# Performance work log

Hardware: AMD Instinct MI355X
Metric: run time of the kernel (lower is better)

The kernel has to match this reference:

```python
import jax, jax.numpy as jnp
import numpy as np

N = 100000
E = 3200000
F_IN = 128
H1, C1 = 2, 16          # conv1: heads=2, out_channels=16, concat -> 32
H2, C2 = 1, 40          # conv2: heads=1, out_channels=num_classes=40
NEG_SLOPE = 0.2


def setup_inputs() -> dict:
    key = jax.random.key(0)
    ks = jax.random.split(key, 12)
    features = jax.random.normal(ks[0], (N, F_IN), dtype=jnp.float32)
    edges = jax.random.randint(ks[1], (2, E), 0, N, dtype=jnp.int64)
    weight = jax.random.uniform(ks[2], (E,), dtype=jnp.float32)  # ignored (edge_dim=None)
    s = 0.1
    W1 = jax.random.normal(ks[3], (F_IN, H1 * C1), dtype=jnp.float32) * s
    att_src1 = jax.random.normal(ks[4], (H1, C1), dtype=jnp.float32) * s
    att_dst1 = jax.random.normal(ks[5], (H1, C1), dtype=jnp.float32) * s
    b1 = jnp.zeros((H1 * C1,), dtype=jnp.float32)
    W2 = jax.random.normal(ks[6], (H1 * C1, H2 * C2), dtype=jnp.float32) * s
    att_src2 = jax.random.normal(ks[7], (H2, C2), dtype=jnp.float32) * s
    att_dst2 = jax.random.normal(ks[8], (H2, C2), dtype=jnp.float32) * s
    b2 = jnp.zeros((H2 * C2,), dtype=jnp.float32)
    return {"features": features, "edges": edges, "weight": weight,
            "W1": W1, "att_src1": att_src1, "att_dst1": att_dst1, "b1": b1,
            "W2": W2, "att_src2": att_src2, "att_dst2": att_dst2, "b2": b2}


def _segment_softmax(e, seg, num_segments):
    # e: [E, H]; softmax over edges sharing the same destination node
    m = jax.ops.segment_max(e, seg, num_segments=num_segments)
    ex = jnp.exp(e - m[seg])
    s = jax.ops.segment_sum(ex, seg, num_segments=num_segments)
    return ex / (s[seg] + 1e-16)


def _gat_conv(x, src, dst, W, att_src, att_dst, bias, heads, out_ch):
    n = x.shape[0]
    h = (x @ W).reshape(n, heads, out_ch)                  # [N,H,C]
    a_src = jnp.sum(h * att_src, axis=-1)                  # [N,H]
    a_dst = jnp.sum(h * att_dst, axis=-1)                  # [N,H]
    e = a_src[src] + a_dst[dst]                            # [E,H]
    e = jnp.where(e > 0, e, NEG_SLOPE * e)                 # LeakyReLU(0.2)
    alpha = _segment_softmax(e, dst, n)                    # [E,H]
    msg = h[src] * alpha[:, :, None]                       # [E,H,C]
    out = jax.ops.segment_sum(msg, dst, num_segments=n)    # [N,H,C]
    return out.reshape(n, heads * out_ch) + bias           # concat=True


def reference(features, edges, weight, W1, att_src1, att_dst1, b1,
              W2, att_src2, att_dst2, b2):
    n = features.shape[0]
    # GATConv default add_self_loops=True (self-loop removal of pre-existing
    # loops skipped: negligible for random edges and not jit-shape-friendly)
    loop = jnp.arange(n, dtype=edges.dtype)
    src = jnp.concatenate([edges[0], loop])
    dst = jnp.concatenate([edges[1], loop])
    x = _gat_conv(features, src, dst, W1, att_src1, att_dst1, b1, H1, C1)
    x = jax.nn.relu(x)
    # F.dropout with training=self.training -> identity in eval mode
    x = _gat_conv(x, src, dst, W2, att_src2, att_dst2, b2, H2, C2)
    return x
```

## Files before the change

kernel.cpp:

```cpp
#include <hip/hip_runtime.h>


#define DEVFN __device__ __forceinline__
#define CB_SHIFT 8
#define CB_SZ 256
#define SC_CHUNK 4096
#define NBMAX 512
#define STASH 12288

DEVFN unsigned short f2h(float f) {
  _Float16 h = (_Float16)f;
  unsigned short u;
  __builtin_memcpy(&u, &h, 2);
  return u;
}
DEVFN float h2f(unsigned short u) {
  _Float16 h;
  __builtin_memcpy(&h, &u, 2);
  return (float)h;
}

DEVFN float lrelu(float e) { return e > 0.f ? e : 0.2f * e; }

DEVFN void acc8(float* acc, float x, uint4 u) {
  acc[0] = fmaf(x, h2f(u.x & 0xffff), acc[0]);
  acc[1] = fmaf(x, h2f(u.x >> 16),    acc[1]);
  acc[2] = fmaf(x, h2f(u.y & 0xffff), acc[2]);
  acc[3] = fmaf(x, h2f(u.y >> 16),    acc[3]);
  acc[4] = fmaf(x, h2f(u.z & 0xffff), acc[4]);
  acc[5] = fmaf(x, h2f(u.z >> 16),    acc[5]);
  acc[6] = fmaf(x, h2f(u.w & 0xffff), acc[6]);
  acc[7] = fmaf(x, h2f(u.w >> 16),    acc[7]);
}

DEVFN void read_edge(const long long* eg64, const int* eg32, int is64, int E,
                     int i, int& s, int& d) {
  if (i >= E) { s = d = i - E; return; }
  if (is64) { s = (int)eg64[i]; d = (int)eg64[E + i]; }
  else      { s = eg32[i];      d = eg32[E + i]; }
}

DEVFN int detect64(const int* eg32, int E, int i0, int t) {
  int base = i0;
  if (base > E - 64) base = E - 64;
  if (base < 0) base = 0;
  int i = base + (t & 63);
  unsigned long long m = __ballot((i < E) && (eg32[2 * i + 1] != 0));
  return m == 0ull;
}

__global__ __launch_bounds__(256) void bucket_hist(const long long* eg64,
                                                   const int* eg32,
                                                   int E, int N, int NB2,
                                                   int* __restrict__ bhist) {
  __shared__ int lh[NBMAX];
  int t = threadIdx.x;
  lh[t] = 0; lh[t + 256] = 0;
  int is64 = detect64(eg32, E, 0, t);
  __syncthreads();
  int EN = E + N;
  int step = (int)gridDim.x * 1024;
  for (int base = (int)blockIdx.x * 1024; base < EN; base += step) {
#pragma unroll
    for (int k = 0; k < 4; k++) {
      int i = base + k * 256 + t;
      if (i < EN) {
        int d;
        if (i >= E) d = i - E;
        else d = is64 ? (int)eg64[E + i] : eg32[E + i];
        atomicAdd(&lh[d >> CB_SHIFT], 1);
      }
    }
  }
  __syncthreads();
  if (t < NB2 && lh[t]) atomicAdd(&bhist[t], lh[t]);
  int t2 = t + 256;
  if (t2 < NB2 && lh[t2]) atomicAdd(&bhist[t2], lh[t2]);
}

__global__ void bucket_scan(const int* __restrict__ bhist,
                            int* __restrict__ bscan, int* __restrict__ gcur,
                            int NB2, int EN) {
  __shared__ int buf[2][NBMAX];
  int t = threadIdx.x;
  int v = (t < NB2) ? bhist[t] : 0;
  buf[0][t] = v;
  __syncthreads();
  int pin = 0;
  for (int off = 1; off < NBMAX; off <<= 1) {
    int nv = buf[pin][t] + (t >= off ? buf[pin][t - off] : 0);
    buf[1 - pin][t] = nv;
    pin ^= 1;
    __syncthreads();
  }
  int excl = buf[pin][t] - v;
  if (t < NB2) { bscan[t] = excl; gcur[t] = excl; }
  if (t == NB2) bscan[t] = EN;
}

__global__ __launch_bounds__(256) void chunk_scatter_sorted(
    const long long* eg64, const int* eg32, int E, int N, int NB2,
    int* __restrict__ gcur, int* __restrict__ tmp) {
  __shared__ int lh[NBMAX];
  __shared__ int lscan[NBMAX];
  __shared__ int lpos[NBMAX];
  __shared__ int gbase[NBMAX];
  __shared__ int sbuf[2][NBMAX];
  __shared__ int payl[SC_CHUNK];
  __shared__ unsigned short bktid[SC_CHUNK];
  int t = threadIdx.x;
  int i0 = (int)blockIdx.x * SC_CHUNK;
  int is64 = detect64(eg32, E, i0, t);
  lh[t] = 0; lh[t + 256] = 0;
  __syncthreads();
  int EN = E + N;
  int i1 = i0 + SC_CHUNK; if (i1 > EN) i1 = EN;
  int total = i1 - i0;
  int es[16], ed[16];
#pragma unroll
  for (int bb = 0; bb < 4; bb++) {
#pragma unroll
    for (int k = 0; k < 4; k++) {
      int idx = bb * 4 + k;
      int i = i0 + bb * 1024 + k * 256 + t;
      int s = 0, d = -1;
      if (i < i1) read_edge(eg64, eg32, is64, E, i, s, d);
      es[idx] = s; ed[idx] = d;
    }
  }
#pragma unroll
  for (int j = 0; j < 16; j++)
    if (ed[j] >= 0) atomicAdd(&lh[ed[j] >> CB_SHIFT], 1);
  __syncthreads();
  sbuf[0][t] = lh[t]; sbuf[0][t + 256] = lh[t + 256];
  __syncthreads();
  int pin = 0;
  for (int off = 1; off < NBMAX; off <<= 1) {
    int nv0 = sbuf[pin][t] + (t >= off ? sbuf[pin][t - off] : 0);
    int nv1 = sbuf[pin][t + 256] + sbuf[pin][t + 256 - off];
    __syncthreads();
    sbuf[1 - pin][t] = nv0; sbuf[1 - pin][t + 256] = nv1;
    pin ^= 1;
    __syncthreads();
  }
  lscan[t] = sbuf[pin][t] - lh[t];
  lscan[t + 256] = sbuf[pin][t + 256] - lh[t + 256];
  lpos[t] = lscan[t]; lpos[t + 256] = lscan[t + 256];
  if (t < NB2 && lh[t]) gbase[t] = atomicAdd(&gcur[t], lh[t]);
  int t2 = t + 256;
  if (t2 < NB2 && lh[t2]) gbase[t2] = atomicAdd(&gcur[t2], lh[t2]);
  __syncthreads();
#pragma unroll
  for (int j = 0; j < 16; j++) {
    if (ed[j] >= 0) {
      int b = ed[j] >> CB_SHIFT;
      int sl = atomicAdd(&lpos[b], 1);
      payl[sl] = (es[j] << CB_SHIFT) | (ed[j] & (CB_SZ - 1));
      bktid[sl] = (unsigned short)b;
    }
  }
  __syncthreads();
  for (int j = t; j < total; j += 256) {
    int b = bktid[j];
    tmp[gbase[b] + (j - lscan[b])] = payl[j];
  }
}

__global__ __launch_bounds__(256) void bucket_rp_sort(const int* __restrict__ bscan,
                                                      const int* __restrict__ tmp,
                                                      int* __restrict__ rp,
                                                      int* __restrict__ csr,
                                                      int N, int EN) {
  __shared__ int lc[CB_SZ];
  __shared__ int ps[256];
  __shared__ int lcur[CB_SZ];
  __shared__ int stash[STASH];
  int b = blockIdx.x, t = threadIdx.x;
  lc[t] = 0;
  __syncthreads();
  int w0 = bscan[b];
  int w1 = bscan[b + 1];
  int cnt = w1 - w0;
  bool fit = (cnt <= STASH);
  int p = w0 + t;
  for (; p + 768 < w1; p += 1024) {
    int e0 = tmp[p], e1 = tmp[p + 256], e2 = tmp[p + 512], e3 = tmp[p + 768];
    if (fit) {
      stash[p - w0] = e0; stash[p - w0 + 256] = e1;
      stash[p - w0 + 512] = e2; stash[p - w0 + 768] = e3;
    }
    atomicAdd(&lc[e0 & (CB_SZ - 1)], 1);
    atomicAdd(&lc[e1 & (CB_SZ - 1)], 1);
    atomicAdd(&lc[e2 & (CB_SZ - 1)], 1);
    atomicAdd(&lc[e3 & (CB_SZ - 1)], 1);
  }
  if (p < w1) {
    bool v1 = p + 256 < w1, v2 = p + 512 < w1;
    int q1 = v1 ? p + 256 : p;
    int q2 = v2 ? p + 512 : p;
    int e0 = tmp[p], e1 = tmp[q1], e2 = tmp[q2];
    if (fit) {
      stash[p - w0] = e0;
      if (v1) stash[q1 - w0] = e1;
      if (v2) stash[q2 - w0] = e2;
    }
    atomicAdd(&lc[e0 & (CB_SZ - 1)], 1);
    if (v1) atomicAdd(&lc[e1 & (CB_SZ - 1)], 1);
    if (v2) atomicAdd(&lc[e2 & (CB_SZ - 1)], 1);
  }
  __syncthreads();
  int a = lc[t];
  ps[t] = a;
  __syncthreads();
  for (int off = 1; off < 256; off <<= 1) {
    int v = ps[t];
    int u = (t >= off) ? ps[t - off] : 0;
    __syncthreads();
    ps[t] = v + u;
    __syncthreads();
  }
  int base = w0 + ps[t] - a;
  lcur[t] = base;
  int n0 = b * CB_SZ;
  if (n0 + t < N) rp[n0 + t] = base;
  if (b == (int)gridDim.x - 1 && t == 0) rp[N] = EN;
  __syncthreads();
  if (fit) {
    for (int j = t; j < cnt; j += 256) {
      int e = stash[j];
      int pos = atomicAdd(&lcur[e & (CB_SZ - 1)], 1);
      csr[pos] = e >> CB_SHIFT;
    }
  } else {
    for (int q = w0 + t; q < w1; q += 256) {
      int e = tmp[q];
      int pos = atomicAdd(&lcur[e & (CB_SZ - 1)], 1);
      csr[pos] = e >> CB_SHIFT;
    }
  }
}

__global__ __launch_bounds__(256) void gemm1f(const float* __restrict__ X,
                                              const float* __restrict__ W,
                                              const float* __restrict__ att_s,
                                              const float* __restrict__ att_d,
                                              uint4* __restrict__ h1h,
                                              float* __restrict__ as1,
                                              float* __restrict__ ad1, int N) {
  __shared__ float Wl[128 * 32];
  __shared__ float Asl[32], Adl[32];
  int t = threadIdx.x;
  for (int i = t; i < 1024; i += 256)
    ((float4*)Wl)[i] = ((const float4*)W)[i];
  if (t < 32) { Asl[t] = att_s[t]; Adl[t] = att_d[t]; }
  __syncthreads();
  int g = t >> 2, j = t & 3;
  int n0 = blockIdx.x * 128 + g * 2;
  int n1 = n0 + 1;
  bool v0 = n0 < N, v1 = n1 < N;
  const float4* X40 = (const float4*)(X + (size_t)n0 * 128);
  const float4* X41 = (const float4*)(X + (size_t)n1 * 128);
  float a0[8], a1[8];
#pragma unroll
  for (int c = 0; c < 8; c++) { a0[c] = 0.f; a1[c] = 0.f; }
  float4 z4 = {0.f, 0.f, 0.f, 0.f};
  for (int k4 = 0; k4 < 32; k4++) {
    float4 x0 = v0 ? X40[k4] : z4;
    float4 x1 = v1 ? X41[k4] : z4;
    const float4* w4 = (const float4*)(Wl + k4 * 128);
    int cb = j * 2;
#pragma unroll
    for (int kr = 0; kr < 4; kr++) {
      float4 wa = w4[kr * 8 + cb];
      float4 wb = w4[kr * 8 + cb + 1];
      float xc0 = kr == 0 ? x0.x : kr == 1 ? x0.y : kr == 2 ? x0.z : x0.w;
      float xc1 = kr == 0 ? x1.x : kr == 1 ? x1.y : kr == 2 ? x1.z : x1.w;
      a0[0] = fmaf(xc0, wa.x, a0[0]); a0[1] = fmaf(xc0, wa.y, a0[1]);
      a0[2] = fmaf(xc0, wa.z, a0[2]); a0[3] = fmaf(xc0, wa.w, a0[3]);
      a0[4] = fmaf(xc0, wb.x, a0[4]); a0[5] = fmaf(xc0, wb.y, a0[5]);
      a0[6] = fmaf(xc0, wb.z, a0[6]); a0[7] = fmaf(xc0, wb.w, a0[7]);
      a1[0] = fmaf(xc1, wa.x, a1[0]); a1[1] = fmaf(xc1, wa.y, a1[1]);
      a1[2] = fmaf(xc1, wa.z, a1[2]); a1[3] = fmaf(xc1, wa.w, a1[3]);
      a1[4] = fmaf(xc1, wb.x, a1[4]); a1[5] = fmaf(xc1, wb.y, a1[5]);
      a1[6] = fmaf(xc1, wb.z, a1[6]); a1[7] = fmaf(xc1, wb.w, a1[7]);
    }
  }
  int ch0 = j * 8;
  float ps0 = 0.f, pd0 = 0.f, ps1 = 0.f, pd1 = 0.f;
#pragma unroll
  for (int c = 0; c < 8; c++) {
    ps0 = fmaf(a0[c], Asl[ch0 + c], ps0);
    pd0 = fmaf(a0[c], Adl[ch0 + c], pd0);
    ps1 = fmaf(a1[c], Asl[ch0 + c], ps1);
    pd1 = fmaf(a1[c], Adl[ch0 + c], pd1);
  }
  ps0 += __shfl_xor(ps0, 1); pd0 += __shfl_xor(pd0, 1);
  ps1 += __shfl_xor(ps1, 1); pd1 += __shfl_xor(pd1, 1);
  float qs0 = __shfl_xor(ps0, 2), qd0 = __shfl_xor(pd0, 2);
  float qs1 = __shfl_xor(ps1, 2), qd1 = __shfl_xor(pd1, 2);
  if (j == 0) {
    if (v0) {
      as1[n0 * 2] = ps0; as1[n0 * 2 + 1] = qs0;
      ad1[n0 * 2] = pd0; ad1[n0 * 2 + 1] = qd0;
    }
    if (v1) {
      as1[n1 * 2] = ps1; as1[n1 * 2 + 1] = qs1;
      ad1[n1 * 2] = pd1; ad1[n1 * 2 + 1] = qd1;
    }
  }
  if (v0) {
    uint4 u;
    u.x = (unsigned)f2h(a0[0]) | ((unsigned)f2h(a0[1]) << 16);
    u.y = (unsigned)f2h(a0[2]) | ((unsigned)f2h(a0[3]) << 16);
    u.z = (unsigned)f2h(a0[4]) | ((unsigned)f2h(a0[5]) << 16);
    u.w = (unsigned)f2h(a0[6]) | ((unsigned)f2h(a0[7]) << 16);
    h1h[(size_t)n0 * 4 + j] = u;
  }
  if (v1) {
    uint4 u;
    u.x = (unsigned)f2h(a1[0]) | ((unsigned)f2h(a1[1]) << 16);
    u.y = (unsigned)f2h(a1[2]) | ((unsigned)f2h(a1[3]) << 16);
    u.z = (unsigned)f2h(a1[4]) | ((unsigned)f2h(a1[5]) << 16);
    u.w = (unsigned)f2h(a1[6]) | ((unsigned)f2h(a1[7]) << 16);
    h1h[(size_t)n1 * 4 + j] = u;
  }
}

__global__ __launch_bounds__(256, 8) void agg1_attn(
    const int* __restrict__ rp, const int* __restrict__ csr,
    const float* __restrict__ as, const float* __restrict__ ad,
    const uint4* __restrict__ h1h, const float* __restrict__ b1,
    const float* __restrict__ W2, const float* __restrict__ as2w,
    const float* __restrict__ ad2w, uint4* __restrict__ x1h,
    float* __restrict__ as2, float* __restrict__ ad2, int N) {
  __shared__ float val[32], vbl[32];
  int t = threadIdx.x;
  if (t < 32) {
    float a = 0.f, b = 0.f;
    for (int c = 0; c < 40; c++) {
      float w = W2[t * 40 + c];
      a = fmaf(w, as2w[c], a);
      b = fmaf(w, ad2w[c], b);
    }
    val[t] = a; vbl[t] = b;
  }
  __syncthreads();
  int nl = t >> 4, r = t & 15;
  int half = r >> 2, cq = r & 3;
  int h = cq >> 1;
  int n = blockIdx.x * 16 + nl;
  float acc[8] = {0, 0, 0, 0, 0, 0, 0, 0};
  float ssum = 0.f;
  if (n < N) {
    int p0 = rp[n], p1 = rp[n + 1];
    float adv = ad[n * 2 + h];
    int p = p0 + half;
    for (; p + 12 < p1; p += 16) {
      int sA = csr[p], sB = csr[p + 4], sC = csr[p + 8], sD = csr[p + 12];
      float eA = as[sA * 2 + h] + adv;
      float eB = as[sB * 2 + h] + adv;
      float eC = as[sC * 2 + h] + adv;
      float eD = as[sD * 2 + h] + adv;
      uint4 uA = h1h[(size_t)sA * 4 + cq];
      uint4 uB = h1h[(size_t)sB * 4 + cq];
      uint4 uC = h1h[(size_t)sC * 4 + cq];
      uint4 uD = h1h[(size_t)sD * 4 + cq];
      float xA = __expf(lrelu(eA));
      float xB = __expf(lrelu(eB));
      float xC = __expf(lrelu(eC));
      float xD = __expf(lrelu(eD));
      ssum += (xA + xB) + (xC + xD);
      acc8(acc, xA, uA);
      acc8(acc, xB, uB);
      acc8(acc, xC, uC);
      acc8(acc, xD, uD);
    }
    if (p < p1) {
      bool vB = p + 4 < p1, vC = p + 8 < p1;
      int pB = vB ? p + 4 : p;
      int pC = vC ? p + 8 : p;
      int sA = csr[p], sB = csr[pB], sC = csr[pC];
      float eA = as[sA * 2 + h] + adv;
      float eB = as[sB * 2 + h] + adv;
      float eC = as[sC * 2 + h] + adv;
      uint4 uA = h1h[(size_t)sA * 4 + cq];
      uint4 uB = h1h[(size_t)sB * 4 + cq];
      uint4 uC = h1h[(size_t)sC * 4 + cq];
      float xA = __expf(lrelu(eA));
      float xB = vB ? __expf(lrelu(eB)) : 0.f;
      float xC = vC ? __expf(lrelu(eC)) : 0.f;
      ssum += xA + xB + xC;
      acc8(acc, xA, uA);
      acc8(acc, xB, uB);
      acc8(acc, xC, uC);
    }
  }
#pragma unroll
  for (int j = 0; j < 8; j++) acc[j] += __shfl_xor(acc[j], 4);
  ssum += __shfl_xor(ssum, 4);
#pragma unroll
  for (int j = 0; j < 8; j++) acc[j] += __shfl_xor(acc[j], 8);
  ssum += __shfl_xor(ssum, 8);
  if (n < N && half == 0) {
    float inv = 1.0f / (ssum + 1e-16f);
    float4 ba = ((const float4*)b1)[cq * 2];
    float4 bb = ((const float4*)b1)[cq * 2 + 1];
    float xv[8];
    xv[0] = fmaxf(fmaf(acc[0], inv, ba.x), 0.f);
    xv[1] = fmaxf(fmaf(acc[1], inv, ba.y), 0.f);
    xv[2] = fmaxf(fmaf(acc[2], inv, ba.z), 0.f);
    xv[3] = fmaxf(fmaf(acc[3], inv, ba.w), 0.f);
    xv[4] = fmaxf(fmaf(acc[4], inv, bb.x), 0.f);
    xv[5] = fmaxf(fmaf(acc[5], inv, bb.y), 0.f);
    xv[6] = fmaxf(fmaf(acc[6], inv, bb.z), 0.f);
    xv[7] = fmaxf(fmaf(acc[7], inv, bb.w), 0.f);
    uint4 u;
    u.x = (unsigned)f2h(xv[0]) | ((unsigned)f2h(xv[1]) << 16);
    u.y = (unsigned)f2h(xv[2]) | ((unsigned)f2h(xv[3]) << 16);
    u.z = (unsigned)f2h(xv[4]) | ((unsigned)f2h(xv[5]) << 16);
    u.w = (unsigned)f2h(xv[6]) | ((unsigned)f2h(xv[7]) << 16);
    x1h[(size_t)n * 4 + cq] = u;
    int ch0 = cq * 8;
    float ss = 0.f, sd = 0.f;
#pragma unroll
    for (int j = 0; j < 8; j++) {
      ss = fmaf(xv[j], val[ch0 + j], ss);
      sd = fmaf(xv[j], vbl[ch0 + j], sd);
    }
    ss += __shfl_xor(ss, 1); sd += __shfl_xor(sd, 1);
    ss += __shfl_xor(ss, 2); sd += __shfl_xor(sd, 2);
    if (cq == 0) { as2[n] = ss; ad2[n] = sd; }
  }
}

__global__ __launch_bounds__(256, 8) void agg2_gemm(
    const int* __restrict__ rp, const int* __restrict__ csr,
    const float* __restrict__ as, const float* __restrict__ ad,
    const uint4* __restrict__ x1h, const float* __restrict__ W2,
    const float* __restrict__ b2, float* __restrict__ outp, int N) {
  __shared__ float Wl[32 * 40];
  __shared__ float xt[16][33];
  __shared__ float hr[16][41];
  int t = threadIdx.x;
  for (int i = t; i < 320; i += 256)
    ((float4*)Wl)[i] = ((const float4*)W2)[i];
  int nl = t >> 4, r = t & 15;
  int half = r >> 2, cq = r & 3;
  int n = blockIdx.x * 16 + nl;
  float acc[8] = {0, 0, 0, 0, 0, 0, 0, 0};
  float ssum = 0.f;
  if (n < N) {
    int p0 = rp[n], p1 = rp[n + 1];
    float adv = ad[n];
    int p = p0 + half;
    for (; p + 12 < p1; p += 16) {
      int sA = csr[p], sB = csr[p + 4], sC = csr[p + 8], sD = csr[p + 12];
      float eA = as[sA] + adv;
      float eB = as[sB] + adv;
      float eC = as[sC] + adv;
      float eD = as[sD] + adv;
      uint4 uA = x1h[(size_t)sA * 4 + cq];
      uint4 uB = x1h[(size_t)sB * 4 + cq];
      uint4 uC = x1h[(size_t)sC * 4 + cq];
      uint4 uD = x1h[(size_t)sD * 4 + cq];
      float xA = __expf(lrelu(eA));
      float xB = __expf(lrelu(eB));
      float xC = __expf(lrelu(eC));
      float xD = __expf(lrelu(eD));
      ssum += (xA + xB) + (xC + xD);
      acc8(acc, xA, uA);
      acc8(acc, xB, uB);
      acc8(acc, xC, uC);
      acc8(acc, xD, uD);
    }
    if (p < p1) {
      bool vB = p + 4 < p1, vC = p + 8 < p1;
      int pB = vB ? p + 4 : p;
      int pC = vC ? p + 8 : p;
      int sA = csr[p], sB = csr[pB], sC = csr[pC];
      float eA = as[sA] + adv;
      float eB = as[sB] + adv;
      float eC = as[sC] + adv;
      uint4 uA = x1h[(size_t)sA * 4 + cq];
      uint4 uB = x1h[(size_t)sB * 4 + cq];
      uint4 uC = x1h[(size_t)sC * 4 + cq];
      float xA = __expf(lrelu(eA));
      float xB = vB ? __expf(lrelu(eB)) : 0.f;
      float xC = vC ? __expf(lrelu(eC)) : 0.f;
      ssum += xA + xB + xC;
      acc8(acc, xA, uA);
      acc8(acc, xB, uB);
      acc8(acc, xC, uC);
    }
  }
#pragma unroll
  for (int j = 0; j < 8; j++) acc[j] += __shfl_xor(acc[j], 4);
  ssum += __shfl_xor(ssum, 4);
#pragma unroll
  for (int j = 0; j < 8; j++) acc[j] += __shfl_xor(acc[j], 8);
  ssum += __shfl_xor(ssum, 8);
  if (n < N && half == 0) {
    float inv = 1.0f / (ssum + 1e-16f);
    int ch0 = cq * 8;
#pragma unroll
    for (int j = 0; j < 8; j++) xt[nl][ch0 + j] = acc[j] * inv;
  }
  __syncthreads();
  if (n < N && r < 8) {
    float a2[5] = {0, 0, 0, 0, 0};
    int cb = r * 5;
    for (int k = 0; k < 32; k++) {
      float x = xt[nl][k];
#pragma unroll
      for (int c = 0; c < 5; c++)
        a2[c] = fmaf(x, Wl[k * 40 + cb + c], a2[c]);
    }
#pragma unroll
    for (int c = 0; c < 5; c++) hr[nl][cb + c] = a2[c];
  }
  __syncthreads();
  if (n < N && r < 10) {
    const float* s = hr[nl] + r * 4;
    float4 bb = ((const float4*)b2)[r];
    float4 v;
    v.x = s[0] + bb.x; v.y = s[1] + bb.y;
    v.z = s[2] + bb.z; v.w = s[3] + bb.w;
    ((float4*)outp)[(size_t)n * 10 + r] = v;
  }
}

extern "C" void kernel_launch(void* const* d_in, const int* in_sizes, int n_in,
                              void* d_out, int out_size, void* d_ws, size_t ws_size,
                              hipStream_t stream) {
  const float* X    = (const float*)d_in[0];
  const long long* eg64 = (const long long*)d_in[1];
  const int* eg32   = (const int*)d_in[1];
  const float* W1   = (const float*)d_in[3];
  const float* as1w = (const float*)d_in[4];
  const float* ad1w = (const float*)d_in[5];
  const float* b1   = (const float*)d_in[6];
  const float* W2   = (const float*)d_in[7];
  const float* as2w = (const float*)d_in[8];
  const float* ad2w = (const float*)d_in[9];
  const float* b2   = (const float*)d_in[10];
  float* out = (float*)d_out;

  const int N  = in_sizes[0] / 128;
  const int E  = in_sizes[1] / 2;
  const int EN = E + N;
  const int NB2 = (N + CB_SZ - 1) / CB_SZ;
  const int NWG = (EN + SC_CHUNK - 1) / SC_CHUNK;

  char* wbase = (char*)d_ws;
  size_t off = 0;
  auto alloc = [&](size_t bytes) -> void* {
    void* p = wbase + off;
    off += (bytes + 255) & ~(size_t)255;
    return p;
  };

  uint4* h1h = (uint4*)alloc((size_t)N * 64);
  size_t usz = (size_t)EN * 4;
  if ((size_t)N * 64 > usz) usz = (size_t)N * 64;
  char* uni = (char*)alloc(usz);
  uint4* x1h = (uint4*)uni;
  int*   tmp = (int*)uni;
  float* as1 = (float*)alloc((size_t)N * 2 * 4);
  float* ad1 = (float*)alloc((size_t)N * 2 * 4);
  float* as2 = (float*)alloc((size_t)N * 4);
  float* ad2 = (float*)alloc((size_t)N * 4);
  int* rp     = (int*)alloc((size_t)(N + 1) * 4);
  int* bhist  = (int*)alloc(NBMAX * 4);
  int* bscan  = (int*)alloc((NBMAX + 1) * 4);
  int* gcur   = (int*)alloc(NBMAX * 4);
  int* csr    = (int*)alloc((size_t)EN * 4);
  (void)ws_size; (void)n_in; (void)out_size;

  const int gN = (N + 127) / 128;

  hipMemsetAsync(bhist, 0, NBMAX * 4, stream);
  bucket_hist<<<1024, 256, 0, stream>>>(eg64, eg32, E, N, NB2, bhist);
  bucket_scan<<<1, NBMAX, 0, stream>>>(bhist, bscan, gcur, NB2, EN);
  chunk_scatter_sorted<<<NWG, 256, 0, stream>>>(eg64, eg32, E, N, NB2, gcur, tmp);
  bucket_rp_sort<<<NB2, 256, 0, stream>>>(bscan, tmp, rp, csr, N, EN);

  gemm1f<<<gN, 256, 0, stream>>>(X, W1, as1w, ad1w, h1h, as1, ad1, N);
  agg1_attn<<<(N + 15) / 16, 256, 0, stream>>>(rp, csr, as1, ad1, h1h, b1,
                                               W2, as2w, ad2w, x1h, as2, ad2, N);
  agg2_gemm<<<(N + 15) / 16, 256, 0, stream>>>(rp, csr, as2, ad2, x1h,
                                               W2, b2, out, N);
}
```

Measured before the change: 326.1 us.

## Fold bucket scan into histogram kernel and co-launch scatter with layer-1 GEMM

The separate single-block bucket_scan kernel is removed. The last histogram block to finish, detected with an atomic counter and thread fences, now performs the prefix scan. The edge scatter and the independent layer-1 GEMM now run in one launch, with blocks split by blockIdx and shared memory overlaid through a union. This saves two kernel launches and lets the compute-bound GEMM overlap the memory-bound scatter. The costs are a larger shared-memory footprint for GEMM blocks, which may lower their occupancy, and the last-block pattern's reliance on correct fence semantics.

```diff
diff --git a/kernel.cpp b/kernel.cpp
--- a/kernel.cpp
+++ b/kernel.cpp
@@ -49,11 +49,13 @@
   return m == 0ull;
 }
 
-__global__ __launch_bounds__(256) void bucket_hist(const long long* eg64,
-                                                   const int* eg32,
-                                                   int E, int N, int NB2,
-                                                   int* __restrict__ bhist) {
+__global__ __launch_bounds__(256) void bucket_hist_scan(
+    const long long* eg64, const int* eg32, int E, int N, int NB2,
+    int* __restrict__ bhist, int* __restrict__ bflag,
+    int* __restrict__ bscan, int* __restrict__ gcur) {
   __shared__ int lh[NBMAX];
+  __shared__ int sbuf[2][NBMAX];
+  __shared__ int lastblk;
   int t = threadIdx.x;
   lh[t] = 0; lh[t + 256] = 0;
   int is64 = detect64(eg32, E, 0, t);
@@ -76,63 +78,15 @@
   if (t < NB2 && lh[t]) atomicAdd(&bhist[t], lh[t]);
   int t2 = t + 256;
   if (t2 < NB2 && lh[t2]) atomicAdd(&bhist[t2], lh[t2]);
-}
-
-__global__ void bucket_scan(const int* __restrict__ bhist,
-                            int* __restrict__ bscan, int* __restrict__ gcur,
-                            int NB2, int EN) {
-  __shared__ int buf[2][NBMAX];
-  int t = threadIdx.x;
-  int v = (t < NB2) ? bhist[t] : 0;
-  buf[0][t] = v;
-  __syncthreads();
-  int pin = 0;
-  for (int off = 1; off < NBMAX; off <<= 1) {
-    int nv = buf[pin][t] + (t >= off ? buf[pin][t - off] : 0);
-    buf[1 - pin][t] = nv;
-    pin ^= 1;
-    __syncthreads();
-  }
-  int excl = buf[pin][t] - v;
-  if (t < NB2) { bscan[t] = excl; gcur[t] = excl; }
-  if (t == NB2) bscan[t] = EN;
-}
-
-__global__ __launch_bounds__(256) void chunk_scatter_sorted(
-    const long long* eg64, const int* eg32, int E, int N, int NB2,
-    int* __restrict__ gcur, int* __restrict__ tmp) {
-  __shared__ int lh[NBMAX];
-  __shared__ int lscan[NBMAX];
-  __shared__ int lpos[NBMAX];
-  __shared__ int gbase[NBMAX];
-  __shared__ int sbuf[2][NBMAX];
-  __shared__ int payl[SC_CHUNK];
-  __shared__ unsigned short bktid[SC_CHUNK];
-  int t = threadIdx.x;
-  int i0 = (int)blockIdx.x * SC_CHUNK;
-  int is64 = detect64(eg32, E, i0, t);
-  lh[t] = 0; lh[t + 256] = 0;
-  __syncthreads();
-  int EN = E + N;
-  int i1 = i0 + SC_CHUNK; if (i1 > EN) i1 = EN;
-  int total = i1 - i0;
-  int es[16], ed[16];
-#pragma unroll
-  for (int bb = 0; bb < 4; bb++) {
-#pragma unroll
-    for (int k = 0; k < 4; k++) {
-      int idx = bb * 4 + k;
-      int i = i0 + bb * 1024 + k * 256 + t;
-      int s = 0, d = -1;
-      if (i < i1) read_edge(eg64, eg32, is64, E, i, s, d);
-      es[idx] = s; ed[idx] = d;
-    }
-  }
-#pragma unroll
-  for (int j = 0; j < 16; j++)
-    if (ed[j] >= 0) atomicAdd(&lh[ed[j] >> CB_SHIFT], 1);
-  __syncthreads();
-  sbuf[0][t] = lh[t]; sbuf[0][t + 256] = lh[t + 256];
+  __threadfence();
+  __syncthreads();
+  if (t == 0) lastblk = (atomicAdd(bflag, 1) == (int)gridDim.x - 1);
+  __syncthreads();
+  if (!lastblk) return;
+  __threadfence();
+  int v0 = (t < NB2) ? bhist[t] : 0;
+  int v1 = (t2 < NB2) ? bhist[t2] : 0;
+  sbuf[0][t] = v0; sbuf[0][t + 256] = v1;
   __syncthreads();
   int pin = 0;
   for (int off = 1; off < NBMAX; off <<= 1) {
@@ -143,26 +97,165 @@
     pin ^= 1;
     __syncthreads();
   }
-  lscan[t] = sbuf[pin][t] - lh[t];
-  lscan[t + 256] = sbuf[pin][t + 256] - lh[t + 256];
-  lpos[t] = lscan[t]; lpos[t + 256] = lscan[t + 256];
-  if (t < NB2 && lh[t]) gbase[t] = atomicAdd(&gcur[t], lh[t]);
-  int t2 = t + 256;
-  if (t2 < NB2 && lh[t2]) gbase[t2] = atomicAdd(&gcur[t2], lh[t2]);
-  __syncthreads();
-#pragma unroll
-  for (int j = 0; j < 16; j++) {
-    if (ed[j] >= 0) {
-      int b = ed[j] >> CB_SHIFT;
-      int sl = atomicAdd(&lpos[b], 1);
-      payl[sl] = (es[j] << CB_SHIFT) | (ed[j] & (CB_SZ - 1));
-      bktid[sl] = (unsigned short)b;
-    }
-  }
-  __syncthreads();
-  for (int j = t; j < total; j += 256) {
-    int b = bktid[j];
-    tmp[gbase[b] + (j - lscan[b])] = payl[j];
+  int e0 = sbuf[pin][t] - v0;
+  int e1 = sbuf[pin][t + 256] - v1;
+  if (t < NB2) { bscan[t] = e0; gcur[t] = e0; }
+  if (t2 < NB2) { bscan[t2] = e1; gcur[t2] = e1; }
+  if (t == 0) bscan[NB2] = EN;
+}
+
+union SMem {
+  struct {
+    int lh[NBMAX]; int lscan[NBMAX]; int lpos[NBMAX]; int gbase[NBMAX];
+    int sbuf[2][NBMAX]; int payl[SC_CHUNK]; unsigned short bktid[SC_CHUNK];
+  } sc;
+  struct {
+    float Wl[128 * 32]; float Asl[32]; float Adl[32];
+  } g1;
+};
+
+__global__ __launch_bounds__(256) void scatter_gemm1(
+    const long long* eg64, const int* eg32, int E, int N, int NB2, int NWG,
+    int* __restrict__ gcur, int* __restrict__ tmp,
+    const float* __restrict__ X, const float* __restrict__ W,
+    const float* __restrict__ att_s, const float* __restrict__ att_d,
+    uint4* __restrict__ h1h, float* __restrict__ as1,
+    float* __restrict__ ad1) {
+  __shared__ SMem sm;
+  int t = threadIdx.x;
+  if ((int)blockIdx.x < NWG) {
+    int i0 = (int)blockIdx.x * SC_CHUNK;
+    int is64 = detect64(eg32, E, i0, t);
+    sm.sc.lh[t] = 0; sm.sc.lh[t + 256] = 0;
+    __syncthreads();
+    int EN = E + N;
+    int i1 = i0 + SC_CHUNK; if (i1 > EN) i1 = EN;
+    int total = i1 - i0;
+    int es[16], ed[16];
+#pragma unroll
+    for (int bb = 0; bb < 4; bb++) {
+#pragma unroll
+      for (int k = 0; k < 4; k++) {
+        int idx = bb * 4 + k;
+        int i = i0 + bb * 1024 + k * 256 + t;
+        int s = 0, d = -1;
+        if (i < i1) read_edge(eg64, eg32, is64, E, i, s, d);
+        es[idx] = s; ed[idx] = d;
+      }
+    }
+#pragma unroll
+    for (int j = 0; j < 16; j++)
+      if (ed[j] >= 0) atomicAdd(&sm.sc.lh[ed[j] >> CB_SHIFT], 1);
+    __syncthreads();
+    sm.sc.sbuf[0][t] = sm.sc.lh[t]; sm.sc.sbuf[0][t + 256] = sm.sc.lh[t + 256];
+    __syncthreads();
+    int pin = 0;
+    for (int off = 1; off < NBMAX; off <<= 1) {
+      int nv0 = sm.sc.sbuf[pin][t] + (t >= off ? sm.sc.sbuf[pin][t - off] : 0);
+      int nv1 = sm.sc.sbuf[pin][t + 256] + sm.sc.sbuf[pin][t + 256 - off];
+      __syncthreads();
+      sm.sc.sbuf[1 - pin][t] = nv0; sm.sc.sbuf[1 - pin][t + 256] = nv1;
+      pin ^= 1;
+      __syncthreads();
+    }
+    sm.sc.lscan[t] = sm.sc.sbuf[pin][t] - sm.sc.lh[t];
+    sm.sc.lscan[t + 256] = sm.sc.sbuf[pin][t + 256] - sm.sc.lh[t + 256];
+    sm.sc.lpos[t] = sm.sc.lscan[t]; sm.sc.lpos[t + 256] = sm.sc.lscan[t + 256];
+    if (t < NB2 && sm.sc.lh[t])
+      sm.sc.gbase[t] = atomicAdd(&gcur[t], sm.sc.lh[t]);
+    int t2 = t + 256;
+    if (t2 < NB2 && sm.sc.lh[t2])
+      sm.sc.gbase[t2] = atomicAdd(&gcur[t2], sm.sc.lh[t2]);
+    __syncthreads();
+#pragma unroll
+    for (int j = 0; j < 16; j++) {
+      if (ed[j] >= 0) {
+        int b = ed[j] >> CB_SHIFT;
+        int sl = atomicAdd(&sm.sc.lpos[b], 1);
+        sm.sc.payl[sl] = (es[j] << CB_SHIFT) | (ed[j] & (CB_SZ - 1));
+        sm.sc.bktid[sl] = (unsigned short)b;
+      }
+    }
+    __syncthreads();
+    for (int j = t; j < total; j += 256) {
+      int b = sm.sc.bktid[j];
+      tmp[sm.sc.gbase[b] + (j - sm.sc.lscan[b])] = sm.sc.payl[j];
+    }
+  } else {
+    for (int i = t; i < 1024; i += 256)
+      ((float4*)sm.g1.Wl)[i] = ((const float4*)W)[i];
+    if (t < 32) { sm.g1.Asl[t] = att_s[t]; sm.g1.Adl[t] = att_d[t]; }
+    __syncthreads();
+    int g = t >> 2, j = t & 3;
+    int n0 = ((int)blockIdx.x - NWG) * 128 + g * 2;
+    int n1 = n0 + 1;
+    bool v0 = n0 < N, v1 = n1 < N;
+    const float4* X40 = (const float4*)(X + (size_t)n0 * 128);
+    const float4* X41 = (const float4*)(X + (size_t)n1 * 128);
+    float a0[8], a1[8];
+#pragma unroll
+    for (int c = 0; c < 8; c++) { a0[c] = 0.f; a1[c] = 0.f; }
+    float4 z4 = {0.f, 0.f, 0.f, 0.f};
+    for (int k4 = 0; k4 < 32; k4++) {
+      float4 x0 = v0 ? X40[k4] : z4;
+      float4 x1 = v1 ? X41[k4] : z4;
+      const float4* w4 = (const float4*)(sm.g1.Wl + k4 * 128);
+      int cb = j * 2;
+#pragma unroll
+      for (int kr = 0; kr < 4; kr++) {
+        float4 wa = w4[kr * 8 + cb];
+        float4 wb = w4[kr * 8 + cb + 1];
+        float xc0 = kr == 0 ? x0.x : kr == 1 ? x0.y : kr == 2 ? x0.z : x0.w;
+        float xc1 = kr == 0 ? x1.x : kr == 1 ? x1.y : kr == 2 ? x1.z : x1.w;
+        a0[0] = fmaf(xc0, wa.x, a0[0]); a0[1] = fmaf(xc0, wa.y, a0[1]);
+        a0[2] = fmaf(xc0, wa.z, a0[2]); a0[3] = fmaf(xc0, wa.w, a0[3]);
+        a0[4] = fmaf(xc0, wb.x, a0[4]); a0[5] = fmaf(xc0, wb.y, a0[5]);
+        a0[6] = fmaf(xc0, wb.z, a0[6]); a0[7] = fmaf(xc0, wb.w, a0[7]);
+        a1[0] = fmaf(xc1, wa.x, a1[0]); a1[1] = fmaf(xc1, wa.y, a1[1]);
+        a1[2] = fmaf(xc1, wa.z, a1[2]); a1[3] = fmaf(xc1, wa.w, a1[3]);
+        a1[4] = fmaf(xc1, wb.x, a1[4]); a1[5] = fmaf(xc1, wb.y, a1[5]);
+        a1[6] = fmaf(xc1, wb.z, a1[6]); a1[7] = fmaf(xc1, wb.w, a1[7]);
+      }
+    }
+    int ch0 = j * 8;
+    float ps0 = 0.f, pd0 = 0.f, ps1 = 0.f, pd1 = 0.f;
+#pragma unroll
+    for (int c = 0; c < 8; c++) {
+      ps0 = fmaf(a0[c], sm.g1.Asl[ch0 + c], ps0);
+      pd0 = fmaf(a0[c], sm.g1.Adl[ch0 + c], pd0);
+      ps1 = fmaf(a1[c], sm.g1.Asl[ch0 + c], ps1);
+      pd1 = fmaf(a1[c], sm.g1.Adl[ch0 + c], pd1);
+    }
+    ps0 += __shfl_xor(ps0, 1); pd0 += __shfl_xor(pd0, 1);
+    ps1 += __shfl_xor(ps1, 1); pd1 += __shfl_xor(pd1, 1);
+    float qs0 = __shfl_xor(ps0, 2), qd0 = __shfl_xor(pd0, 2);
+    float qs1 = __shfl_xor(ps1, 2), qd1 = __shfl_xor(pd1, 2);
+    if (j == 0) {
+      if (v0) {
+        as1[n0 * 2] = ps0; as1[n0 * 2 + 1] = qs0;
+        ad1[n0 * 2] = pd0; ad1[n0 * 2 + 1] = qd0;
+      }
+      if (v1) {
+        as1[n1 * 2] = ps1; as1[n1 * 2 + 1] = qs1;
+        ad1[n1 * 2] = pd1; ad1[n1 * 2 + 1] = qd1;
+      }
+    }
+    if (v0) {
+      uint4 u;
+      u.x = (unsigned)f2h(a0[0]) | ((unsigned)f2h(a0[1]) << 16);
+      u.y = (unsigned)f2h(a0[2]) | ((unsigned)f2h(a0[3]) << 16);
+      u.z = (unsigned)f2h(a0[4]) | ((unsigned)f2h(a0[5]) << 16);
+      u.w = (unsigned)f2h(a0[6]) | ((unsigned)f2h(a0[7]) << 16);
+      h1h[(size_t)n0 * 4 + j] = u;
+    }
+    if (v1) {
+      uint4 u;
+      u.x = (unsigned)f2h(a1[0]) | ((unsigned)f2h(a1[1]) << 16);
+      u.y = (unsigned)f2h(a1[2]) | ((unsigned)f2h(a1[3]) << 16);
+      u.z = (unsigned)f2h(a1[4]) | ((unsigned)f2h(a1[5]) << 16);
+      u.w = (unsigned)f2h(a1[6]) | ((unsigned)f2h(a1[7]) << 16);
+      h1h[(size_t)n1 * 4 + j] = u;
+    }
   }
 }
 
@@ -237,92 +330,6 @@
       int pos = atomicAdd(&lcur[e & (CB_SZ - 1)], 1);
       csr[pos] = e >> CB_SHIFT;
     }
-  }
-}
-
-__global__ __launch_bounds__(256) void gemm1f(const float* __restrict__ X,
-                                              const float* __restrict__ W,
-                                              const float* __restrict__ att_s,
-                                              const float* __restrict__ att_d,
-                                              uint4* __restrict__ h1h,
-                                              float* __restrict__ as1,
-                                              float* __restrict__ ad1, int N) {
-  __shared__ float Wl[128 * 32];
-  __shared__ float Asl[32], Adl[32];
-  int t = threadIdx.x;
-  for (int i = t; i < 1024; i += 256)
-    ((float4*)Wl)[i] = ((const float4*)W)[i];
-  if (t < 32) { Asl[t] = att_s[t]; Adl[t] = att_d[t]; }
-  __syncthreads();
-  int g = t >> 2, j = t & 3;
-  int n0 = blockIdx.x * 128 + g * 2;
-  int n1 = n0 + 1;
-  bool v0 = n0 < N, v1 = n1 < N;
-  const float4* X40 = (const float4*)(X + (size_t)n0 * 128);
-  const float4* X41 = (const float4*)(X + (size_t)n1 * 128);
-  float a0[8], a1[8];
-#pragma unroll
-  for (int c = 0; c < 8; c++) { a0[c] = 0.f; a1[c] = 0.f; }
-  float4 z4 = {0.f, 0.f, 0.f, 0.f};
-  for (int k4 = 0; k4 < 32; k4++) {
-    float4 x0 = v0 ? X40[k4] : z4;
-    float4 x1 = v1 ? X41[k4] : z4;
-    const float4* w4 = (const float4*)(Wl + k4 * 128);
-    int cb = j * 2;
-#pragma unroll
-    for (int kr = 0; kr < 4; kr++) {
-      float4 wa = w4[kr * 8 + cb];
-      float4 wb = w4[kr * 8 + cb + 1];
-      float xc0 = kr == 0 ? x0.x : kr == 1 ? x0.y : kr == 2 ? x0.z : x0.w;
-      float xc1 = kr == 0 ? x1.x : kr == 1 ? x1.y : kr == 2 ? x1.z : x1.w;
-      a0[0] = fmaf(xc0, wa.x, a0[0]); a0[1] = fmaf(xc0, wa.y, a0[1]);
-      a0[2] = fmaf(xc0, wa.z, a0[2]); a0[3] = fmaf(xc0, wa.w, a0[3]);
-      a0[4] = fmaf(xc0, wb.x, a0[4]); a0[5] = fmaf(xc0, wb.y, a0[5]);
-      a0[6] = fmaf(xc0, wb.z, a0[6]); a0[7] = fmaf(xc0, wb.w, a0[7]);
-      a1[0] = fmaf(xc1, wa.x, a1[0]); a1[1] = fmaf(xc1, wa.y, a1[1]);
-      a1[2] = fmaf(xc1, wa.z, a1[2]); a1[3] = fmaf(xc1, wa.w, a1[3]);
-      a1[4] = fmaf(xc1, wb.x, a1[4]); a1[5] = fmaf(xc1, wb.y, a1[5]);
-      a1[6] = fmaf(xc1, wb.z, a1[6]); a1[7] = fmaf(xc1, wb.w, a1[7]);
-    }
-  }
-  int ch0 = j * 8;
-  float ps0 = 0.f, pd0 = 0.f, ps1 = 0.f, pd1 = 0.f;
-#pragma unroll
-  for (int c = 0; c < 8; c++) {
-    ps0 = fmaf(a0[c], Asl[ch0 + c], ps0);
-    pd0 = fmaf(a0[c], Adl[ch0 + c], pd0);
-    ps1 = fmaf(a1[c], Asl[ch0 + c], ps1);
-    pd1 = fmaf(a1[c], Adl[ch0 + c], pd1);
-  }
-  ps0 += __shfl_xor(ps0, 1); pd0 += __shfl_xor(pd0, 1);
-  ps1 += __shfl_xor(ps1, 1); pd1 += __shfl_xor(pd1, 1);
-  float qs0 = __shfl_xor(ps0, 2), qd0 = __shfl_xor(pd0, 2);
-  float qs1 = __shfl_xor(ps1, 2), qd1 = __shfl_xor(pd1, 2);
-  if (j == 0) {
-    if (v0) {
-      as1[n0 * 2] = ps0; as1[n0 * 2 + 1] = qs0;
-      ad1[n0 * 2] = pd0; ad1[n0 * 2 + 1] = qd0;
-    }
-    if (v1) {
-      as1[n1 * 2] = ps1; as1[n1 * 2 + 1] = qs1;
-      ad1[n1 * 2] = pd1; ad1[n1 * 2 + 1] = qd1;
-    }
-  }
-  if (v0) {
-    uint4 u;
-    u.x = (unsigned)f2h(a0[0]) | ((unsigned)f2h(a0[1]) << 16);
-    u.y = (unsigned)f2h(a0[2]) | ((unsigned)f2h(a0[3]) << 16);
-    u.z = (unsigned)f2h(a0[4]) | ((unsigned)f2h(a0[5]) << 16);
-    u.w = (unsigned)f2h(a0[6]) | ((unsigned)f2h(a0[7]) << 16);
-    h1h[(size_t)n0 * 4 + j] = u;
-  }
-  if (v1) {
-    uint4 u;
-    u.x = (unsigned)f2h(a1[0]) | ((unsigned)f2h(a1[1]) << 16);
-    u.y = (unsigned)f2h(a1[2]) | ((unsigned)f2h(a1[3]) << 16);
-    u.z = (unsigned)f2h(a1[4]) | ((unsigned)f2h(a1[5]) << 16);
-    u.w = (unsigned)f2h(a1[6]) | ((unsigned)f2h(a1[7]) << 16);
-    h1h[(size_t)n1 * 4 + j] = u;
   }
 }
 
@@ -570,7 +577,7 @@
   float* as2 = (float*)alloc((size_t)N * 4);
   float* ad2 = (float*)alloc((size_t)N * 4);
   int* rp     = (int*)alloc((size_t)(N + 1) * 4);
-  int* bhist  = (int*)alloc(NBMAX * 4);
+  int* bhist  = (int*)alloc((NBMAX + 1) * 4);
   int* bscan  = (int*)alloc((NBMAX + 1) * 4);
   int* gcur   = (int*)alloc(NBMAX * 4);
   int* csr    = (int*)alloc((size_t)EN * 4);
@@ -578,13 +585,14 @@
 
   const int gN = (N + 127) / 128;
 
-  hipMemsetAsync(bhist, 0, NBMAX * 4, stream);
-  bucket_hist<<<1024, 256, 0, stream>>>(eg64, eg32, E, N, NB2, bhist);
-  bucket_scan<<<1, NBMAX, 0, stream>>>(bhist, bscan, gcur, NB2, EN);
-  chunk_scatter_sorted<<<NWG, 256, 0, stream>>>(eg64, eg32, E, N, NB2, gcur, tmp);
+  hipMemsetAsync(bhist, 0, (NBMAX + 1) * 4, stream);
+  bucket_hist_scan<<<1024, 256, 0, stream>>>(eg64, eg32, E, N, NB2,
+                                             bhist, bhist + NBMAX, bscan, gcur);
+  scatter_gemm1<<<NWG + gN, 256, 0, stream>>>(eg64, eg32, E, N, NB2, NWG,
+                                              gcur, tmp, X, W1, as1w, ad1w,
+                                              h1h, as1, ad1);
   bucket_rp_sort<<<NB2, 256, 0, stream>>>(bscan, tmp, rp, csr, N, EN);
 
-  gemm1f<<<gN, 256, 0, stream>>>(X, W1, as1w, ad1w, h1h, as1, ad1, N);
   agg1_attn<<<(N + 15) / 16, 256, 0, stream>>>(rp, csr, as1, ad1, h1h, b1,
                                                W2, as2w, ad2w, x1h, as2, ad2, N);
   agg2_gemm<<<(N + 15) / 16, 256, 0, stream>>>(rp, csr, as2, ad2, x1h,
```

New measurement: 365.6 us. 12.1% more time.
